# Performance work log

Measured on AMD Instinct MI355X. Metric: run time of the kernel, lower is better.

The kernel has to match this reference:

```python
import jax, jax.numpy as jnp
import numpy as np
from jax.scipy.linalg import solve_triangular

B, N = 8192, 1024  # patch batch, neighborhood size; order=3 -> 10 jet coefficients


def setup_inputs() -> dict:
    key = jax.random.key(0)
    k1, k2 = jax.random.split(key)
    points = jax.random.normal(k1, (B, 3, N), dtype=jnp.float32)
    weights = jax.random.uniform(k2, (B, N), dtype=jnp.float32)
    return {"points": points, "weights": weights}


def fit_wjet_order3(points, weights):
    # points: [B,3,N], weights: [B,N]
    bsz, _, n = points.shape
    x = points[:, 0, :, None]  # [B,N,1]
    y = points[:, 1, :, None]
    z = points[:, 2, :, None]
    w = weights[:, :, None]                      # [B,N,1]
    valid_count = jnp.sum(w > 0.001, axis=1)     # [B,1]
    w_vec = jnp.where(valid_count > 18, weights, jnp.ones_like(weights))[:, :, None]  # [B,N,1]

    # scale normalization h (order > 1 branch)
    h = (jnp.mean(jnp.abs(x), axis=1) + jnp.mean(jnp.abs(y), axis=1)) / 2.0  # [B,1]
    h = jnp.where(jnp.abs(h) < 0.0001, 0.1, h)
    hh = h[:, :, None]                            # [B,1,1]
    x = x / hh
    y = y / hh

    # order-3 polynomial feature matrix A: [B,N,10]
    x_2 = x * x
    y_2 = y * y
    xy = x * y
    A = jnp.concatenate([x, y, x_2, y_2, xy, x_2 * x, y_2 * y, x_2 * y, y_2 * x,
                         jnp.ones_like(x)], axis=2)
    h_2 = h * h
    h_3 = h_2 * h
    d_inv = 1.0 / jnp.concatenate([h, h, h_2, h_2, h_2, h_3, h_3, h_3, h_3,
                                   jnp.ones_like(h)], axis=1)  # [B,10]

    # normal equations (weighted): XtX [B,10,10], XtY [B,10,1]
    XtX = jnp.einsum('bnm,bnk->bmk', A, w_vec * A)
    XtY = jnp.einsum('bnm,bnk->bmk', A, w_vec * z)

    # batched Cholesky solve (happy path of solve_linear_system)
    L = jnp.linalg.cholesky(XtX)
    u = solve_triangular(L, XtY, lower=True)
    beta = solve_triangular(jnp.swapaxes(L, -1, -2), u, lower=False)  # [B,10,1]

    beta = d_inv[:, :, None] * beta  # D_inv @ beta (D_inv is diagonal)

    ones_b1 = jnp.ones((bsz, 1), dtype=beta.dtype)
    n_est = jnp.concatenate([-beta[:, 0:2, 0], ones_b1], axis=1)
    n_est = n_est / jnp.linalg.norm(n_est, axis=1, keepdims=True)

    # analytic neighbor normals (order == 3)
    def bk(k):
        return beta[:, k][:, None, :]  # [B,1,1] broadcasts over N
    nx = -(bk(0) + 2 * bk(2) * x + bk(4) * y + 3 * bk(5) * x_2 + 2 * bk(7) * xy + bk(8) * y_2)
    ny = -(bk(1) + 2 * bk(3) * y + bk(4) * x + 3 * bk(6) * y_2 + bk(7) * x_2 + 2 * bk(8) * xy)
    nn_ = jnp.concatenate([nx, ny, jnp.ones((bsz, n, 1), dtype=beta.dtype)], axis=2)  # [B,N,3]
    neighbor_normals = nn_ / jnp.linalg.norm(nn_, axis=2, keepdims=True)

    return beta[:, :, 0], n_est, neighbor_normals


def reference(points, weights):
    return fit_wjet_order3(points, weights)
```

## Files before the change

kernel.cpp:

```cpp
#include <hip/hip_runtime.h>
#include <math.h>

#define NPTS 1024
#define THREADS 256

typedef float v2f __attribute__((ext_vector_type(2)));
typedef int v2i __attribute__((ext_vector_type(2)));

static __device__ __forceinline__ v2f b2(float s) { return (v2f){s, s}; }
static __device__ __forceinline__ v2f vabs2(v2f v) {
  v2i u = __builtin_bit_cast(v2i, v);
  u &= (v2i){0x7fffffff, 0x7fffffff};
  return __builtin_bit_cast(v2f, u);
}

template <int CTRL>
__device__ __forceinline__ float dpp_add(float v) {
  int m = __builtin_amdgcn_update_dpp(0, __builtin_bit_cast(int, v), CTRL, 0xF, 0xF, true);
  return v + __builtin_bit_cast(float, m);
}

__device__ __forceinline__ float row_red16(float v) {
  v = dpp_add<0x111>(v);
  v = dpp_add<0x112>(v);
  v = dpp_add<0x114>(v);
  v = dpp_add<0x118>(v);
  return v;
}

__device__ __forceinline__ float rl_f32(float v, int l) {
  return __builtin_bit_cast(float,
      __builtin_amdgcn_readlane(__builtin_bit_cast(int, v), l));
}

__device__ __forceinline__ float bperm_f(int srclane, float v) {
  return __builtin_bit_cast(float,
      __builtin_amdgcn_ds_bpermute(srclane << 2, __builtin_bit_cast(int, v)));
}

__device__ __forceinline__ float fast_rsq(float x) {
#if __has_builtin(__builtin_amdgcn_rsqf)
  return __builtin_amdgcn_rsqf(x);
#else
  return 1.0f / sqrtf(x);
#endif
}

__device__ __forceinline__ float rcp_nr(float d) {
#if __has_builtin(__builtin_amdgcn_rcpf)
  float r = __builtin_amdgcn_rcpf(d);
  return r * (2.0f - d * r);
#else
  return 1.0f / d;
#endif
}

__global__ void __launch_bounds__(THREADS) deepfit_kernel(
    const float* __restrict__ pts, const float* __restrict__ wts,
    float* __restrict__ beta_out, float* __restrict__ nest_out,
    float* __restrict__ nn_out)
{
  const int b = blockIdx.x;
  const int t = threadIdx.x;
  const int lane = t & 63;
  const int wid = t >> 6;

  __shared__ float s_red[16][40];
  __shared__ int s_cnt[4];
  __shared__ float s_Lf[100];
  __shared__ float s_bh[11];

  const float4* px4 = reinterpret_cast<const float4*>(pts + (size_t)b * (3 * NPTS));
  const float4* pw4 = reinterpret_cast<const float4*>(wts + (size_t)b * NPTS);

  float4 lx4 = px4[t];
  float4 ly4 = px4[THREADS + t];
  float4 lz4 = px4[2 * THREADS + t];
  float4 lw4 = pw4[t];

  v2f xp[2] = {{lx4.x, lx4.y}, {lx4.z, lx4.w}};
  v2f yq[2] = {{ly4.x, ly4.y}, {ly4.z, ly4.w}};
  v2f zp[2] = {{lz4.x, lz4.y}, {lz4.z, lz4.w}};
  v2f wp[2] = {{lw4.x, lw4.y}, {lw4.z, lw4.w}};

  const int part = wid * 4 + (lane >> 4);

  v2f hab2 = vabs2(xp[0]) + vabs2(yq[0]) + vabs2(xp[1]) + vabs2(yq[1]);
  int cnt = 0;
  cnt += (int)__popcll(__ballot(lw4.x > 0.001f));
  cnt += (int)__popcll(__ballot(lw4.y > 0.001f));
  cnt += (int)__popcll(__ballot(lw4.z > 0.001f));
  cnt += (int)__popcll(__ballot(lw4.w > 0.001f));
  {
    float habs = row_red16(hab2.x + hab2.y);
    if ((lane & 15) == 15) s_red[part][39] = habs;
    if (lane == 0) s_cnt[wid] = cnt;
  }

  float momvec = 0.f;
  bool wone = false;
  for (int it = 0; it < 2; ++it) {
    if (it == 1) __syncthreads();
    v2f M2[28], Z2[10];
#pragma unroll
    for (int i = 0; i < 28; ++i) M2[i] = b2(0.f);
#pragma unroll
    for (int i = 0; i < 10; ++i) Z2[i] = b2(0.f);

#pragma unroll
    for (int q = 0; q < 2; ++q) {
      v2f x = xp[q], y = yq[q];
      v2f w = wone ? b2(1.0f) : wp[q];
      v2f wz = w * zp[q];
      v2f y1 = y, y2 = y * y, y3 = y2 * y, y4 = y3 * y, y5 = y4 * y, y6 = y5 * y;
      v2f tx = w;
      M2[0] += tx;          M2[1] += tx * y1; M2[2] += tx * y2; M2[3] += tx * y3;
      M2[4] += tx * y4;     M2[5] += tx * y5; M2[6] += tx * y6;
      tx *= x;
      M2[7] += tx;          M2[8] += tx * y1; M2[9] += tx * y2; M2[10] += tx * y3;
      M2[11] += tx * y4;    M2[12] += tx * y5;
      tx *= x;
      M2[13] += tx;         M2[14] += tx * y1; M2[15] += tx * y2; M2[16] += tx * y3;
      M2[17] += tx * y4;
      tx *= x;
      M2[18] += tx;         M2[19] += tx * y1; M2[20] += tx * y2; M2[21] += tx * y3;
      tx *= x;
      M2[22] += tx;         M2[23] += tx * y1; M2[24] += tx * y2;
      tx *= x;
      M2[25] += tx;         M2[26] += tx * y1;
      tx *= x;
      M2[27] += tx;
      v2f tz = wz;
      Z2[0] += tz;          Z2[1] += tz * y1; Z2[2] += tz * y2; Z2[3] += tz * y3;
      tz *= x;
      Z2[4] += tz;          Z2[5] += tz * y1; Z2[6] += tz * y2;
      tz *= x;
      Z2[7] += tz;          Z2[8] += tz * y1;
      tz *= x;
      Z2[9] += tz;
    }

#pragma unroll
    for (int i = 0; i < 28; ++i) {
      float v = row_red16(M2[i].x + M2[i].y);
      if ((lane & 15) == 15) s_red[part][i] = v;
    }
#pragma unroll
    for (int i = 0; i < 10; ++i) {
      float v = row_red16(Z2[i].x + Z2[i].y);
      if ((lane & 15) == 15) s_red[part][28 + i] = v;
    }
    __syncthreads();

    if (wid == 0 && lane < 40) {
      float acc = 0.f;
#pragma unroll
      for (int j = 0; j < 16; ++j) acc += s_red[j][lane];
      momvec = acc;
    }
    int ctot = s_cnt[0] + s_cnt[1] + s_cnt[2] + s_cnt[3];
    if (it == 1 || ctot > 18) break;
    wone = true;
  }

  if (wid == 0) {
    float mh;
    {
      float htot = rl_f32(momvec, 39);
      mh = htot * (1.0f / 2048.0f);
      if (fabsf(mh) < 1e-4f) mh = 0.1f;
    }
    const int lc = (lane < 10) ? lane : 0;
    const int axi = (0x18D21u >> (2 * lc)) & 3;
    const int ayi = (0x27184u >> (2 * lc)) & 3;
    constexpr int AXC[10] = {1, 0, 2, 0, 1, 3, 0, 2, 1, 0};
    constexpr int AYC[10] = {0, 1, 0, 2, 1, 0, 3, 1, 2, 0};
    float a[10], yy;
#pragma unroll
    for (int j = 0; j < 10; ++j) {
      int as = axi + AXC[j];
      int bs = ayi + AYC[j];
      int idx = as * 7 - (as * (as - 1)) / 2 + bs;
      a[j] = bperm_f(idx, momvec);
    }
    {
      int zi = axi * 4 - (axi * (axi - 1)) / 2 + ayi;
      yy = bperm_f(28 + zi, momvec);
    }

    float bf = 0.f;
    if (lane < 10) {
      float rd_own = 1.0f;
#pragma unroll
      for (int j = 0; j < 10; ++j) {
        float dj = rl_f32(a[j], j);
        float rdj = rcp_nr(dj);
        float lij = a[j] * rdj;
        s_Lf[lane * 10 + j] = lij;
        if (lane == j) rd_own = rdj;
        float wj = rl_f32(yy, j);
        if (lane > j) yy -= lij * wj;
#pragma unroll
        for (int k = j + 1; k < 10; ++k) {
          float ajk = rl_f32(a[k], j);
          a[k] -= lij * ajk;
        }
      }
      yy *= rd_own;
      asm volatile("s_waitcnt lgkmcnt(0)" ::: "memory");
      __builtin_amdgcn_sched_barrier(0);
#pragma unroll
      for (int j = 9; j >= 0; --j) {
        float xj = rl_f32(yy, j);
        if (lane < j) yy -= s_Lf[j * 10 + lane] * xj;
      }
      bf = yy;
      s_bh[lane] = bf;
      beta_out[(size_t)b * 10 + lane] = bf;
    }
    if (lane == 0) {
      s_bh[10] = mh;
      float b0 = rl_f32(bf, 0);
      float b1 = rl_f32(bf, 1);
      float invn = fast_rsq(b0 * b0 + b1 * b1 + 1.0f);
      nest_out[(size_t)b * 3 + 0] = -b0 * invn;
      nest_out[(size_t)b * 3 + 1] = -b1 * invn;
      nest_out[(size_t)b * 3 + 2] = invn;
    }
  }
  __syncthreads();

  float bb[10];
#pragma unroll
  for (int j = 0; j < 10; ++j) bb[j] = s_bh[j];
  const float mh = s_bh[10];
  const float ih = 1.0f / mh;
  const float ih2 = ih * ih;
  const float u0 = bb[0], u2 = 2.f * bb[2] * ih, u4 = bb[4] * ih;
  const float u5 = 3.f * bb[5] * ih2, u7 = 2.f * bb[7] * ih2, u8 = bb[8] * ih2;
  const float v1 = bb[1], v3 = 2.f * bb[3] * ih, v4 = bb[4] * ih;
  const float v6 = 3.f * bb[6] * ih2, v7 = bb[7] * ih2, v8 = 2.f * bb[8] * ih2;

  float nx[4], ny[4], nz[4];
#pragma unroll
  for (int q = 0; q < 2; ++q) {
    v2f x = xp[q], y = yq[q];
    v2f x2 = x * x, y2 = y * y, xy = x * y;
    v2f sx = b2(u0) + b2(u2) * x + b2(u4) * y + b2(u5) * x2 + b2(u7) * xy + b2(u8) * y2;
    v2f sy = b2(v1) + b2(v3) * y + b2(v4) * x + b2(v6) * y2 + b2(v7) * x2 + b2(v8) * xy;
    v2f vx = -sx, vy = -sy;
    v2f n2 = vx * vx + vy * vy + b2(1.0f);
    float i0 = fast_rsq(n2.x), i1 = fast_rsq(n2.y);
    nx[2 * q + 0] = vx.x * i0; ny[2 * q + 0] = vy.x * i0; nz[2 * q + 0] = i0;
    nx[2 * q + 1] = vx.y * i1; ny[2 * q + 1] = vy.y * i1; nz[2 * q + 1] = i1;
  }
  {
    float4* o4 = reinterpret_cast<float4*>(nn_out + (size_t)b * (NPTS * 3));
    float4 f0 = make_float4(nx[0], ny[0], nz[0], nx[1]);
    float4 f1 = make_float4(ny[1], nz[1], nx[2], ny[2]);
    float4 f2 = make_float4(nz[2], nx[3], ny[3], nz[3]);
    o4[3 * t + 0] = f0;
    o4[3 * t + 1] = f1;
    o4[3 * t + 2] = f2;
  }
}

extern "C" void kernel_launch(void* const* d_in, const int* in_sizes, int n_in,
                              void* d_out, int out_size, void* d_ws, size_t ws_size,
                              hipStream_t stream) {
  const float* pts = (const float*)d_in[0];
  const float* wts = (const float*)d_in[1];
  float* out = (float*)d_out;
  const int B = in_sizes[1] / NPTS;
  float* beta_out = out;
  float* nest_out = out + (size_t)B * 10;
  float* nn_out = out + (size_t)B * 13;
  deepfit_kernel<<<B, THREADS, 0, stream>>>(pts, wts, beta_out, nest_out, nn_out);
}
```

Before: 45.19 us.

## Process each patch with a single wavefront and drop block barriers

Each 1024-point patch now goes to one 64-thread wavefront instead of a 256-thread block. Every lane handles 16 points and accumulates the moment sums in scalar registers. The reductions use DPP plus a small shared buffer read back by the same wave, which removes all __syncthreads and the cross-wave reduction. The weight-fallback pass is now a direct branch that reloads z. The cost is more registers per thread, and the packed two-wide math used for accumulation is lost, in a kernel that is probably bound by memory bandwidth.

```diff
diff --git a/kernel.cpp b/kernel.cpp
--- a/kernel.cpp
+++ b/kernel.cpp
@@ -2,17 +2,11 @@
 #include <math.h>
 
 #define NPTS 1024
-#define THREADS 256
 
 typedef float v2f __attribute__((ext_vector_type(2)));
 typedef int v2i __attribute__((ext_vector_type(2)));
 
 static __device__ __forceinline__ v2f b2(float s) { return (v2f){s, s}; }
-static __device__ __forceinline__ v2f vabs2(v2f v) {
-  v2i u = __builtin_bit_cast(v2i, v);
-  u &= (v2i){0x7fffffff, 0x7fffffff};
-  return __builtin_bit_cast(v2f, u);
-}
 
 template <int CTRL>
 __device__ __forceinline__ float dpp_add(float v) {
@@ -55,185 +49,193 @@
 #endif
 }
 
-__global__ void __launch_bounds__(THREADS) deepfit_kernel(
+__device__ __forceinline__ void acc_pt(float M[28], float Z[10],
+                                       float x, float y, float w, float z) {
+  float wz = w * z;
+  float y1 = y, y2 = y * y, y3 = y2 * y, y4 = y3 * y, y5 = y4 * y, y6 = y5 * y;
+  float tx = w;
+  M[0] += tx; M[1] += tx * y1; M[2] += tx * y2; M[3] += tx * y3;
+  M[4] += tx * y4; M[5] += tx * y5; M[6] += tx * y6;
+  tx *= x;
+  M[7] += tx; M[8] += tx * y1; M[9] += tx * y2; M[10] += tx * y3;
+  M[11] += tx * y4; M[12] += tx * y5;
+  tx *= x;
+  M[13] += tx; M[14] += tx * y1; M[15] += tx * y2; M[16] += tx * y3;
+  M[17] += tx * y4;
+  tx *= x;
+  M[18] += tx; M[19] += tx * y1; M[20] += tx * y2; M[21] += tx * y3;
+  tx *= x;
+  M[22] += tx; M[23] += tx * y1; M[24] += tx * y2;
+  tx *= x;
+  M[25] += tx; M[26] += tx * y1;
+  tx *= x;
+  M[27] += tx;
+  float tz = wz;
+  Z[0] += tz; Z[1] += tz * y1; Z[2] += tz * y2; Z[3] += tz * y3;
+  tz *= x;
+  Z[4] += tz; Z[5] += tz * y1; Z[6] += tz * y2;
+  tz *= x;
+  Z[7] += tz; Z[8] += tz * y1;
+  tz *= x;
+  Z[9] += tz;
+}
+
+__global__ void __launch_bounds__(64) deepfit_kernel(
     const float* __restrict__ pts, const float* __restrict__ wts,
     float* __restrict__ beta_out, float* __restrict__ nest_out,
     float* __restrict__ nn_out)
 {
   const int b = blockIdx.x;
-  const int t = threadIdx.x;
-  const int lane = t & 63;
-  const int wid = t >> 6;
-
-  __shared__ float s_red[16][40];
-  __shared__ int s_cnt[4];
+  const int lane = threadIdx.x;
+
+  __shared__ float s_part[4][40];
   __shared__ float s_Lf[100];
-  __shared__ float s_bh[11];
 
   const float4* px4 = reinterpret_cast<const float4*>(pts + (size_t)b * (3 * NPTS));
   const float4* pw4 = reinterpret_cast<const float4*>(wts + (size_t)b * NPTS);
 
-  float4 lx4 = px4[t];
-  float4 ly4 = px4[THREADS + t];
-  float4 lz4 = px4[2 * THREADS + t];
-  float4 lw4 = pw4[t];
-
-  v2f xp[2] = {{lx4.x, lx4.y}, {lx4.z, lx4.w}};
-  v2f yq[2] = {{ly4.x, ly4.y}, {ly4.z, ly4.w}};
-  v2f zp[2] = {{lz4.x, lz4.y}, {lz4.z, lz4.w}};
-  v2f wp[2] = {{lw4.x, lw4.y}, {lw4.z, lw4.w}};
-
-  const int part = wid * 4 + (lane >> 4);
-
-  v2f hab2 = vabs2(xp[0]) + vabs2(yq[0]) + vabs2(xp[1]) + vabs2(yq[1]);
+  float4 xc[4], yc[4];
+  float M[28], Z[10];
+#pragma unroll
+  for (int i = 0; i < 28; ++i) M[i] = 0.f;
+#pragma unroll
+  for (int i = 0; i < 10; ++i) Z[i] = 0.f;
+  float habs = 0.f;
   int cnt = 0;
-  cnt += (int)__popcll(__ballot(lw4.x > 0.001f));
-  cnt += (int)__popcll(__ballot(lw4.y > 0.001f));
-  cnt += (int)__popcll(__ballot(lw4.z > 0.001f));
-  cnt += (int)__popcll(__ballot(lw4.w > 0.001f));
+
+#pragma unroll
+  for (int c = 0; c < 4; ++c) {
+    xc[c] = px4[lane + 64 * c];
+    yc[c] = px4[256 + lane + 64 * c];
+    float4 z4 = px4[512 + lane + 64 * c];
+    float4 w4 = pw4[lane + 64 * c];
+    float xs[4] = {xc[c].x, xc[c].y, xc[c].z, xc[c].w};
+    float ys[4] = {yc[c].x, yc[c].y, yc[c].z, yc[c].w};
+    float zs[4] = {z4.x, z4.y, z4.z, z4.w};
+    float ws[4] = {w4.x, w4.y, w4.z, w4.w};
+#pragma unroll
+    for (int p = 0; p < 4; ++p) {
+      habs += fabsf(xs[p]) + fabsf(ys[p]);
+      cnt += (int)__popcll(__ballot(ws[p] > 0.001f));
+    }
+#pragma unroll
+    for (int p = 0; p < 4; ++p) acc_pt(M, Z, xs[p], ys[p], ws[p], zs[p]);
+  }
+
+  const int grp = lane >> 4;
+  const bool gw = ((lane & 15) == 15);
+#pragma unroll
+  for (int i = 0; i < 28; ++i) {
+    float v = row_red16(M[i]);
+    if (gw) s_part[grp][i] = v;
+  }
+#pragma unroll
+  for (int i = 0; i < 10; ++i) {
+    float v = row_red16(Z[i]);
+    if (gw) s_part[grp][28 + i] = v;
+  }
   {
-    float habs = row_red16(hab2.x + hab2.y);
-    if ((lane & 15) == 15) s_red[part][39] = habs;
-    if (lane == 0) s_cnt[wid] = cnt;
-  }
-
+    float v = row_red16(habs);
+    if (gw) s_part[grp][38] = v;
+  }
   float momvec = 0.f;
-  bool wone = false;
-  for (int it = 0; it < 2; ++it) {
-    if (it == 1) __syncthreads();
-    v2f M2[28], Z2[10];
-#pragma unroll
-    for (int i = 0; i < 28; ++i) M2[i] = b2(0.f);
-#pragma unroll
-    for (int i = 0; i < 10; ++i) Z2[i] = b2(0.f);
-
-#pragma unroll
-    for (int q = 0; q < 2; ++q) {
-      v2f x = xp[q], y = yq[q];
-      v2f w = wone ? b2(1.0f) : wp[q];
-      v2f wz = w * zp[q];
-      v2f y1 = y, y2 = y * y, y3 = y2 * y, y4 = y3 * y, y5 = y4 * y, y6 = y5 * y;
-      v2f tx = w;
-      M2[0] += tx;          M2[1] += tx * y1; M2[2] += tx * y2; M2[3] += tx * y3;
-      M2[4] += tx * y4;     M2[5] += tx * y5; M2[6] += tx * y6;
-      tx *= x;
-      M2[7] += tx;          M2[8] += tx * y1; M2[9] += tx * y2; M2[10] += tx * y3;
-      M2[11] += tx * y4;    M2[12] += tx * y5;
-      tx *= x;
-      M2[13] += tx;         M2[14] += tx * y1; M2[15] += tx * y2; M2[16] += tx * y3;
-      M2[17] += tx * y4;
-      tx *= x;
-      M2[18] += tx;         M2[19] += tx * y1; M2[20] += tx * y2; M2[21] += tx * y3;
-      tx *= x;
-      M2[22] += tx;         M2[23] += tx * y1; M2[24] += tx * y2;
-      tx *= x;
-      M2[25] += tx;         M2[26] += tx * y1;
-      tx *= x;
-      M2[27] += tx;
-      v2f tz = wz;
-      Z2[0] += tz;          Z2[1] += tz * y1; Z2[2] += tz * y2; Z2[3] += tz * y3;
-      tz *= x;
-      Z2[4] += tz;          Z2[5] += tz * y1; Z2[6] += tz * y2;
-      tz *= x;
-      Z2[7] += tz;          Z2[8] += tz * y1;
-      tz *= x;
-      Z2[9] += tz;
-    }
-
+  if (lane < 39)
+    momvec = (s_part[0][lane] + s_part[1][lane]) +
+             (s_part[2][lane] + s_part[3][lane]);
+
+  if (cnt <= 18) {
+#pragma unroll
+    for (int i = 0; i < 28; ++i) M[i] = 0.f;
+#pragma unroll
+    for (int i = 0; i < 10; ++i) Z[i] = 0.f;
+    for (int c = 0; c < 4; ++c) {
+      float4 z4 = px4[512 + lane + 64 * c];
+      float xs[4] = {xc[c].x, xc[c].y, xc[c].z, xc[c].w};
+      float ys[4] = {yc[c].x, yc[c].y, yc[c].z, yc[c].w};
+      float zs[4] = {z4.x, z4.y, z4.z, z4.w};
+#pragma unroll
+      for (int p = 0; p < 4; ++p) acc_pt(M, Z, xs[p], ys[p], 1.0f, zs[p]);
+    }
 #pragma unroll
     for (int i = 0; i < 28; ++i) {
-      float v = row_red16(M2[i].x + M2[i].y);
-      if ((lane & 15) == 15) s_red[part][i] = v;
+      float v = row_red16(M[i]);
+      if (gw) s_part[grp][i] = v;
     }
 #pragma unroll
     for (int i = 0; i < 10; ++i) {
-      float v = row_red16(Z2[i].x + Z2[i].y);
-      if ((lane & 15) == 15) s_red[part][28 + i] = v;
-    }
-    __syncthreads();
-
-    if (wid == 0 && lane < 40) {
-      float acc = 0.f;
-#pragma unroll
-      for (int j = 0; j < 16; ++j) acc += s_red[j][lane];
-      momvec = acc;
-    }
-    int ctot = s_cnt[0] + s_cnt[1] + s_cnt[2] + s_cnt[3];
-    if (it == 1 || ctot > 18) break;
-    wone = true;
-  }
-
-  if (wid == 0) {
-    float mh;
-    {
-      float htot = rl_f32(momvec, 39);
-      mh = htot * (1.0f / 2048.0f);
-      if (fabsf(mh) < 1e-4f) mh = 0.1f;
-    }
-    const int lc = (lane < 10) ? lane : 0;
-    const int axi = (0x18D21u >> (2 * lc)) & 3;
-    const int ayi = (0x27184u >> (2 * lc)) & 3;
-    constexpr int AXC[10] = {1, 0, 2, 0, 1, 3, 0, 2, 1, 0};
-    constexpr int AYC[10] = {0, 1, 0, 2, 1, 0, 3, 1, 2, 0};
-    float a[10], yy;
+      float v = row_red16(Z[i]);
+      if (gw) s_part[grp][28 + i] = v;
+    }
+    if (lane < 38)
+      momvec = (s_part[0][lane] + s_part[1][lane]) +
+               (s_part[2][lane] + s_part[3][lane]);
+  }
+
+  float mh;
+  {
+    float htot = rl_f32(momvec, 38);
+    mh = htot * (1.0f / 2048.0f);
+    if (fabsf(mh) < 1e-4f) mh = 0.1f;
+  }
+
+  const int lc = (lane < 10) ? lane : 0;
+  const int axi = (0x18D21u >> (2 * lc)) & 3;
+  const int ayi = (0x27184u >> (2 * lc)) & 3;
+  constexpr int AXC[10] = {1, 0, 2, 0, 1, 3, 0, 2, 1, 0};
+  constexpr int AYC[10] = {0, 1, 0, 2, 1, 0, 3, 1, 2, 0};
+  float a[10], yy;
+#pragma unroll
+  for (int j = 0; j < 10; ++j) {
+    int as = axi + AXC[j];
+    int bs = ayi + AYC[j];
+    int idx = as * 7 - (as * (as - 1)) / 2 + bs;
+    a[j] = bperm_f(idx, momvec);
+  }
+  {
+    int zi = axi * 4 - (axi * (axi - 1)) / 2 + ayi;
+    yy = bperm_f(28 + zi, momvec);
+  }
+
+  float bf = 0.f;
+  if (lane < 10) {
+    float rd_own = 1.0f;
 #pragma unroll
     for (int j = 0; j < 10; ++j) {
-      int as = axi + AXC[j];
-      int bs = ayi + AYC[j];
-      int idx = as * 7 - (as * (as - 1)) / 2 + bs;
-      a[j] = bperm_f(idx, momvec);
-    }
-    {
-      int zi = axi * 4 - (axi * (axi - 1)) / 2 + ayi;
-      yy = bperm_f(28 + zi, momvec);
-    }
-
-    float bf = 0.f;
-    if (lane < 10) {
-      float rd_own = 1.0f;
-#pragma unroll
-      for (int j = 0; j < 10; ++j) {
-        float dj = rl_f32(a[j], j);
-        float rdj = rcp_nr(dj);
-        float lij = a[j] * rdj;
-        s_Lf[lane * 10 + j] = lij;
-        if (lane == j) rd_own = rdj;
-        float wj = rl_f32(yy, j);
-        if (lane > j) yy -= lij * wj;
-#pragma unroll
-        for (int k = j + 1; k < 10; ++k) {
-          float ajk = rl_f32(a[k], j);
-          a[k] -= lij * ajk;
-        }
+      float dj = rl_f32(a[j], j);
+      float rdj = rcp_nr(dj);
+      float lij = a[j] * rdj;
+      s_Lf[lane * 10 + j] = lij;
+      if (lane == j) rd_own = rdj;
+      float wj = rl_f32(yy, j);
+      if (lane > j) yy -= lij * wj;
+#pragma unroll
+      for (int k = j + 1; k < 10; ++k) {
+        float ajk = rl_f32(a[k], j);
+        a[k] -= lij * ajk;
       }
-      yy *= rd_own;
-      asm volatile("s_waitcnt lgkmcnt(0)" ::: "memory");
-      __builtin_amdgcn_sched_barrier(0);
-#pragma unroll
-      for (int j = 9; j >= 0; --j) {
-        float xj = rl_f32(yy, j);
-        if (lane < j) yy -= s_Lf[j * 10 + lane] * xj;
-      }
-      bf = yy;
-      s_bh[lane] = bf;
-      beta_out[(size_t)b * 10 + lane] = bf;
-    }
-    if (lane == 0) {
-      s_bh[10] = mh;
-      float b0 = rl_f32(bf, 0);
-      float b1 = rl_f32(bf, 1);
-      float invn = fast_rsq(b0 * b0 + b1 * b1 + 1.0f);
-      nest_out[(size_t)b * 3 + 0] = -b0 * invn;
-      nest_out[(size_t)b * 3 + 1] = -b1 * invn;
-      nest_out[(size_t)b * 3 + 2] = invn;
-    }
-  }
-  __syncthreads();
+    }
+    yy *= rd_own;
+    asm volatile("s_waitcnt lgkmcnt(0)" ::: "memory");
+    __builtin_amdgcn_sched_barrier(0);
+#pragma unroll
+    for (int j = 9; j >= 0; --j) {
+      float xj = rl_f32(yy, j);
+      if (lane < j) yy -= s_Lf[j * 10 + lane] * xj;
+    }
+    bf = yy;
+    beta_out[(size_t)b * 10 + lane] = bf;
+  }
 
   float bb[10];
 #pragma unroll
-  for (int j = 0; j < 10; ++j) bb[j] = s_bh[j];
-  const float mh = s_bh[10];
+  for (int j = 0; j < 10; ++j) bb[j] = rl_f32(bf, j);
+  if (lane == 0) {
+    float b0 = bb[0], b1 = bb[1];
+    float invn = fast_rsq(b0 * b0 + b1 * b1 + 1.0f);
+    nest_out[(size_t)b * 3 + 0] = -b0 * invn;
+    nest_out[(size_t)b * 3 + 1] = -b1 * invn;
+    nest_out[(size_t)b * 3 + 2] = invn;
+  }
   const float ih = 1.0f / mh;
   const float ih2 = ih * ih;
   const float u0 = bb[0], u2 = 2.f * bb[2] * ih, u4 = bb[4] * ih;
@@ -241,27 +243,28 @@
   const float v1 = bb[1], v3 = 2.f * bb[3] * ih, v4 = bb[4] * ih;
   const float v6 = 3.f * bb[6] * ih2, v7 = bb[7] * ih2, v8 = 2.f * bb[8] * ih2;
 
-  float nx[4], ny[4], nz[4];
-#pragma unroll
-  for (int q = 0; q < 2; ++q) {
-    v2f x = xp[q], y = yq[q];
-    v2f x2 = x * x, y2 = y * y, xy = x * y;
-    v2f sx = b2(u0) + b2(u2) * x + b2(u4) * y + b2(u5) * x2 + b2(u7) * xy + b2(u8) * y2;
-    v2f sy = b2(v1) + b2(v3) * y + b2(v4) * x + b2(v6) * y2 + b2(v7) * x2 + b2(v8) * xy;
-    v2f vx = -sx, vy = -sy;
-    v2f n2 = vx * vx + vy * vy + b2(1.0f);
-    float i0 = fast_rsq(n2.x), i1 = fast_rsq(n2.y);
-    nx[2 * q + 0] = vx.x * i0; ny[2 * q + 0] = vy.x * i0; nz[2 * q + 0] = i0;
-    nx[2 * q + 1] = vx.y * i1; ny[2 * q + 1] = vy.y * i1; nz[2 * q + 1] = i1;
-  }
-  {
-    float4* o4 = reinterpret_cast<float4*>(nn_out + (size_t)b * (NPTS * 3));
-    float4 f0 = make_float4(nx[0], ny[0], nz[0], nx[1]);
-    float4 f1 = make_float4(ny[1], nz[1], nx[2], ny[2]);
-    float4 f2 = make_float4(nz[2], nx[3], ny[3], nz[3]);
-    o4[3 * t + 0] = f0;
-    o4[3 * t + 1] = f1;
-    o4[3 * t + 2] = f2;
+  float4* o4 = reinterpret_cast<float4*>(nn_out + (size_t)b * (NPTS * 3));
+#pragma unroll
+  for (int c = 0; c < 4; ++c) {
+    v2f xpr[2] = {{xc[c].x, xc[c].y}, {xc[c].z, xc[c].w}};
+    v2f ypr[2] = {{yc[c].x, yc[c].y}, {yc[c].z, yc[c].w}};
+    float nx[4], ny[4], nz[4];
+#pragma unroll
+    for (int q = 0; q < 2; ++q) {
+      v2f x = xpr[q], y = ypr[q];
+      v2f x2 = x * x, y2 = y * y, xy = x * y;
+      v2f sx = b2(u0) + b2(u2) * x + b2(u4) * y + b2(u5) * x2 + b2(u7) * xy + b2(u8) * y2;
+      v2f sy = b2(v1) + b2(v3) * y + b2(v4) * x + b2(v6) * y2 + b2(v7) * x2 + b2(v8) * xy;
+      v2f vx = -sx, vy = -sy;
+      v2f n2 = vx * vx + vy * vy + b2(1.0f);
+      float i0 = fast_rsq(n2.x), i1 = fast_rsq(n2.y);
+      nx[2 * q + 0] = vx.x * i0; ny[2 * q + 0] = vy.x * i0; nz[2 * q + 0] = i0;
+      nx[2 * q + 1] = vx.y * i1; ny[2 * q + 1] = vy.y * i1; nz[2 * q + 1] = i1;
+    }
+    int base = 3 * (lane + 64 * c);
+    o4[base + 0] = make_float4(nx[0], ny[0], nz[0], nx[1]);
+    o4[base + 1] = make_float4(ny[1], nz[1], nx[2], ny[2]);
+    o4[base + 2] = make_float4(nz[2], nx[3], ny[3], nz[3]);
   }
 }
 
@@ -275,5 +278,5 @@
   float* beta_out = out;
   float* nest_out = out + (size_t)B * 10;
   float* nn_out = out + (size_t)B * 13;
-  deepfit_kernel<<<B, THREADS, 0, stream>>>(pts, wts, beta_out, nest_out, nn_out);
-}
+  deepfit_kernel<<<B, 64, 0, stream>>>(pts, wts, beta_out, nest_out, nn_out);
+}
```

Result: slower. 50.71 us (+12.2%).
